# Kernel optimization log

Hardware: AMD Instinct MI355X
Metric: run time of the kernel (lower is better)

The kernel has to match this reference:

```python
import jax, jax.numpy as jnp
import numpy as np

N, D, B, O, E = 4096, 1024, 512, 1, 16  # samples, in_size, bottleneck, out_size, n_tasks
L1_LAMBDA = 1e-4


def setup_inputs() -> dict:
    key = jax.random.key(0)
    ks = jax.random.split(key, 6)
    x = jax.random.normal(ks[0], (N, D), jnp.float32)
    keys = jax.random.randint(ks[1], (N,), 0, E, dtype=jnp.int32)
    W1 = jax.random.normal(ks[2], (E, B, D), jnp.float32) / np.sqrt(D).astype(np.float32)
    b1 = jax.random.normal(ks[3], (E, B), jnp.float32) * 0.01
    W2 = jax.random.normal(ks[4], (E, O, B), jnp.float32) / np.sqrt(B).astype(np.float32)
    b2 = jax.random.normal(ks[5], (E, O), jnp.float32) * 0.01
    return {"x": x, "keys": keys, "W1": W1, "b1": b1, "W2": W2, "b2": b2}


def reference(x, keys, W1, b1, W2, b2):
    """Per-sample task-specific 2-layer bottleneck MLP dispatch.

    x: [N, D] float; keys: [N] int task indices.
    W1: [E, B, D], b1: [E, B], W2: [E, O, B], b2: [E, O].
    Returns (out [N, O], l1_lambda * sum_n L1(params of expert keys[n])).
    """
    n = x.shape[0]
    e = W1.shape[0]
    # Dense MoE dispatch: first linear for all experts, then select per sample.
    h_all = jnp.einsum('nd,ebd->neb', x, W1) + b1[None]          # [N, E, B]
    h = h_all[jnp.arange(n), keys]                                # [N, B]
    h = jax.nn.relu(h)                                            # activation='relu'
    out = jnp.einsum('nb,nob->no', h, W2[keys]) + b2[keys]        # [N, O]
    # L1 of the selected expert's parameters is accumulated once per sample.
    l1_per_expert = (jnp.abs(W1).sum((1, 2)) + jnp.abs(b1).sum(1)
                     + jnp.abs(W2).sum((1, 2)) + jnp.abs(b2).sum(1))  # [E]
    counts = jnp.zeros((e,), x.dtype).at[keys].add(jnp.ones((), x.dtype))
    l1 = jnp.asarray(L1_LAMBDA, x.dtype) * jnp.dot(counts, l1_per_expert)
    return out, l1
```

## Files before the change

### kernel.cpp

```cpp
#include <hip/hip_runtime.h>
#include <hip/hip_bf16.h>

#define N_S 4096
#define D_IN 1024
#define B_BOT 512
#define E_EXP 16
#define L1_LAMBDA 1e-4f

#define MT 64
#define NT 128
#define KC 64
#define MT_GRID 6
#define IDSTR 512

typedef float f32x4 __attribute__((ext_vector_type(4)));
typedef short bf16x8 __attribute__((ext_vector_type(8)));
typedef unsigned int u32;


__device__ __forceinline__ ushort4 cvt4(float4 v) {
    union { __hip_bfloat162 b2[2]; ushort4 u4; } u;
    u.b2[0] = __float22bfloat162_rn({v.x, v.y});
    u.b2[1] = __float22bfloat162_rn({v.z, v.w});
    return u.u4;
}

__device__ __forceinline__ void async16(const ushort* g, ushort* l) {
    __builtin_amdgcn_global_load_lds(
        (const __attribute__((address_space(1))) u32*)g,
        (__attribute__((address_space(3))) u32*)l, 16, 0, 0);
}

__global__ __launch_bounds__(256)
void prep_kernel(const float* __restrict__ x, const int* __restrict__ keys,
                 const float* __restrict__ W1, const float* __restrict__ b1,
                 const float* __restrict__ W2, const float* __restrict__ b2,
                 float* __restrict__ out, int* __restrict__ counts,
                 float* __restrict__ l1small, float* __restrict__ l1part,
                 int* __restrict__ ids, ushort* __restrict__ W1b,
                 ushort* __restrict__ xb) {
    const int blk = blockIdx.x;
    const int t = threadIdx.x;
    if (blk < E_EXP) {
        const int e = blk;
        out[e * 256 + t] = 0.f;
        float s = fabsf(b1[e * B_BOT + t]) + fabsf(b1[e * B_BOT + 256 + t])
                + fabsf(W2[e * B_BOT + t]) + fabsf(W2[e * B_BOT + 256 + t]);
        if (t == 0) s += fabsf(b2[e]);
#pragma unroll
        for (int off = 32; off > 0; off >>= 1) s += __shfl_down(s, off);
        __shared__ float ws4a[4];
        __shared__ int cnt_s;
        if ((t & 63) == 0) ws4a[t >> 6] = s;
        if (t == 0) cnt_s = 0;
        __syncthreads();
        if (t == 0) l1small[e] = ws4a[0] + ws4a[1] + ws4a[2] + ws4a[3];
        const int lane = t & 63;
        for (int it = 0; it < N_S / 256; ++it) {
            const int i = it * 256 + t;
            const bool m = (keys[i] == e);
            const unsigned long long mask = __ballot(m);
            int base = 0;
            if (lane == 0) base = atomicAdd(&cnt_s, __popcll(mask));
            base = __shfl(base, 0);
            if (m) {
                const int pos = base + __popcll(mask & ((1ull << lane) - 1ull));
                if (pos < IDSTR) ids[e * IDSTR + pos] = i;
            }
        }
        __syncthreads();
        if (t == 0) counts[e] = min(cnt_s, IDSTR);
    } else if (blk < E_EXP + 1024) {
        const int i = blk - E_EXP;
        const long long base = (long long)i * 2048;
        const float4* __restrict__ src = (const float4*)W1;
        ushort4* __restrict__ dst = (ushort4*)W1b;
        float s = 0.f;
#pragma unroll
        for (int m = 0; m < 8; ++m) {
            const long long idx = base + m * 256 + t;
            float4 v = src[idx];
            s += fabsf(v.x) + fabsf(v.y) + fabsf(v.z) + fabsf(v.w);
            dst[idx] = cvt4(v);
        }
#pragma unroll
        for (int off = 32; off > 0; off >>= 1) s += __shfl_down(s, off);
        __shared__ float ws4b[4];
        if ((t & 63) == 0) ws4b[t >> 6] = s;
        __syncthreads();
        if (t == 0) l1part[i] = ws4b[0] + ws4b[1] + ws4b[2] + ws4b[3];
    } else {
        const int i = blk - E_EXP - 1024;
        const long long base = (long long)i * 2048;
        const float4* __restrict__ src = (const float4*)x;
        ushort4* __restrict__ dst = (ushort4*)xb;
#pragma unroll
        for (int m = 0; m < 8; ++m) {
            const long long idx = base + m * 256 + t;
            dst[idx] = cvt4(src[idx]);
        }
    }
}

__global__ __launch_bounds__(256, 2)
void mlp_kernel(const ushort* __restrict__ W1b, const ushort* __restrict__ xb,
                const float* __restrict__ b1, const float* __restrict__ W2,
                const float* __restrict__ b2, const int* __restrict__ counts,
                const float* __restrict__ l1small, const float* __restrict__ l1part,
                const int* __restrict__ ids, float* __restrict__ out) {
    const int b = blockIdx.x;
    const int mt = b >> 6, e = (b & 63) >> 2, nb = b & 3;
    const int t = threadIdx.x, wave = t >> 6, lane = t & 63;
    const int l15 = lane & 15, qd = lane >> 4;
    const int wm = wave & 1, wn = wave >> 1;

    __shared__ __align__(16) ushort As[MT * KC];
    __shared__ __align__(16) ushort Bs[NT * KC];
    __shared__ int sid_s[MT];
    __shared__ float red[2][MT];

    if (b == 0 && wave == 0) {
        const int el = lane >> 2, sub = lane & 3;
        float s = 0.f;
#pragma unroll
        for (int k = 0; k < 16; ++k) s += l1part[el * 64 + sub * 16 + k];
        s += __shfl_xor(s, 1);
        s += __shfl_xor(s, 2);
        float v = (sub == 0) ? (float)counts[el] * (s + l1small[el]) : 0.f;
        v += __shfl_xor(v, 4);
        v += __shfl_xor(v, 8);
        v += __shfl_xor(v, 16);
        v += __shfl_xor(v, 32);
        if (lane == 0) out[N_S] = L1_LAMBDA * v;
    }

    const int cnt = counts[e];
    const int m0 = mt * MT;
    if (m0 >= cnt) return;

    if (t < MT) sid_s[t] = ids[e * IDSTR + min(m0 + t, cnt - 1)];
    __syncthreads();

    const int colb = nb * NT;
    float b1v[4], w2v[4];
#pragma unroll
    for (int j = 0; j < 4; ++j) {
        const int col = colb + 64 * wn + 16 * j + l15;
        b1v[j] = b1[e * B_BOT + col];
        w2v[j] = W2[e * B_BOT + col];
    }
    const float b2e = b2[e];

    const ushort* gA[2];
    ushort* dA[2];
#pragma unroll
    for (int p = 0; p < 2; ++p) {
        const int u = p * 256 + t, r = u >> 3;
        const int q = (u & 7) ^ (r & 7);
        gA[p] = xb + (size_t)sid_s[r] * D_IN + q * 8;
        dA[p] = As + (size_t)(p * 256 + wave * 64) * 8;
    }
    const ushort* gB[4];
    ushort* dB[4];
#pragma unroll
    for (int p = 0; p < 4; ++p) {
        const int u = p * 256 + t, r = u >> 3;
        const int q = (u & 7) ^ (r & 7);
        gB[p] = W1b + (size_t)(e * B_BOT + colb + r) * D_IN + q * 8;
        dB[p] = Bs + (size_t)(p * 256 + wave * 64) * 8;
    }

    const ushort* fA[2][2];
#pragma unroll
    for (int i = 0; i < 2; ++i)
#pragma unroll
        for (int s = 0; s < 2; ++s) {
            const int r = 32 * wm + 16 * i + l15;
            fA[i][s] = As + (size_t)(r * 8 + ((s * 4 + qd) ^ (r & 7))) * 8;
        }
    const ushort* fB[4][2];
#pragma unroll
    for (int j = 0; j < 4; ++j)
#pragma unroll
        for (int s = 0; s < 2; ++s) {
            const int r = 64 * wn + 16 * j + l15;
            fB[j][s] = Bs + (size_t)(r * 8 + ((s * 4 + qd) ^ (r & 7))) * 8;
        }

    f32x4 acc[2][4];
#pragma unroll
    for (int i = 0; i < 2; ++i)
#pragma unroll
        for (int j = 0; j < 4; ++j) acc[i][j] = (f32x4){0.f, 0.f, 0.f, 0.f};

    for (int c = 0; c < D_IN / KC; ++c) {
        const int ko = c * KC;
        __syncthreads();
#pragma unroll
        for (int p = 0; p < 2; ++p) async16(gA[p] + ko, dA[p]);
#pragma unroll
        for (int p = 0; p < 4; ++p) async16(gB[p] + ko, dB[p]);
        __syncthreads();
#pragma unroll
        for (int s = 0; s < 2; ++s) {
            bf16x8 a0 = *(const bf16x8*)fA[0][s];
            bf16x8 a1 = *(const bf16x8*)fA[1][s];
            bf16x8 bb[4];
#pragma unroll
            for (int j = 0; j < 4; ++j) bb[j] = *(const bf16x8*)fB[j][s];
#pragma unroll
            for (int j = 0; j < 4; ++j) {
                acc[0][j] = __builtin_amdgcn_mfma_f32_16x16x32_bf16(a0, bb[j], acc[0][j], 0, 0, 0);
                acc[1][j] = __builtin_amdgcn_mfma_f32_16x16x32_bf16(a1, bb[j], acc[1][j], 0, 0, 0);
            }
        }
    }

    float p[2][4] = {{0.f, 0.f, 0.f, 0.f}, {0.f, 0.f, 0.f, 0.f}};
#pragma unroll
    for (int j = 0; j < 4; ++j)
#pragma unroll
        for (int i = 0; i < 2; ++i)
#pragma unroll
            for (int r = 0; r < 4; ++r) {
                const float h = fmaxf(acc[i][j][r] + b1v[j], 0.f);
                p[i][r] = fmaf(h, w2v[j], p[i][r]);
            }
#pragma unroll
    for (int off = 8; off > 0; off >>= 1)
#pragma unroll
        for (int i = 0; i < 2; ++i)
#pragma unroll
            for (int r = 0; r < 4; ++r) p[i][r] += __shfl_xor(p[i][r], off, 16);

    if (l15 == 0) {
#pragma unroll
        for (int i = 0; i < 2; ++i)
#pragma unroll
            for (int r = 0; r < 4; ++r)
                red[wn][32 * wm + 16 * i + 4 * qd + r] = p[i][r];
    }
    __syncthreads();
    if (t < MT) {
        const int m = m0 + t;
        if (m < cnt) {
            float v = red[0][t] + red[1][t];
            if (nb == 0) v += b2e;
            atomicAdd(&out[ids[e * IDSTR + m]], v);
        }
    }
}

extern "C" void kernel_launch(void* const* d_in, const int* in_sizes, int n_in,
                              void* d_out, int out_size, void* d_ws, size_t ws_size,
                              hipStream_t stream) {
    const float* x    = (const float*)d_in[0];
    const int*   keys = (const int*)d_in[1];
    const float* W1   = (const float*)d_in[2];
    const float* b1   = (const float*)d_in[3];
    const float* W2   = (const float*)d_in[4];
    const float* b2   = (const float*)d_in[5];
    float* out = (float*)d_out;

    char* ws = (char*)d_ws;
    int*    counts  = (int*)(ws + 0);
    float*  l1small = (float*)(ws + 64);
    float*  l1part  = (float*)(ws + 128);
    int*    ids     = (int*)(ws + 4224);
    ushort* W1b     = (ushort*)(ws + 65536);
    ushort* xb      = (ushort*)(ws + 65536 + 16777216);

    prep_kernel<<<E_EXP + 1024 + 512, 256, 0, stream>>>(
        x, keys, W1, b1, W2, b2, out, counts, l1small, l1part, ids, W1b, xb);
    mlp_kernel<<<MT_GRID * 64, 256, 0, stream>>>(
        W1b, xb, b1, W2, b2, counts, l1small, l1part, ids, out);
}
```

Before: 115.7 us.

## Double-buffer LDS tiles to overlap async global loads with MFMA compute

```diff
diff --git a/kernel.cpp b/kernel.cpp
--- a/kernel.cpp
+++ b/kernel.cpp
@@ -114,8 +114,10 @@
     const int l15 = lane & 15, qd = lane >> 4;
     const int wm = wave & 1, wn = wave >> 1;
 
-    __shared__ __align__(16) ushort As[MT * KC];
-    __shared__ __align__(16) ushort Bs[NT * KC];
+    __shared__ __align__(16) ushort As0[MT * KC];
+    __shared__ __align__(16) ushort As1[MT * KC];
+    __shared__ __align__(16) ushort Bs0[NT * KC];
+    __shared__ __align__(16) ushort Bs1[NT * KC];
     __shared__ int sid_s[MT];
     __shared__ float red[2][MT];
 
@@ -152,39 +154,37 @@
     const float b2e = b2[e];
 
     const ushort* gA[2];
-    ushort* dA[2];
+    const int dldsA[2] = {(0 * 256 + wave * 64) * 8, (1 * 256 + wave * 64) * 8};
 #pragma unroll
     for (int p = 0; p < 2; ++p) {
         const int u = p * 256 + t, r = u >> 3;
         const int q = (u & 7) ^ (r & 7);
         gA[p] = xb + (size_t)sid_s[r] * D_IN + q * 8;
-        dA[p] = As + (size_t)(p * 256 + wave * 64) * 8;
     }
     const ushort* gB[4];
-    ushort* dB[4];
+    int dldsB[4];
 #pragma unroll
     for (int p = 0; p < 4; ++p) {
         const int u = p * 256 + t, r = u >> 3;
         const int q = (u & 7) ^ (r & 7);
         gB[p] = W1b + (size_t)(e * B_BOT + colb + r) * D_IN + q * 8;
-        dB[p] = Bs + (size_t)(p * 256 + wave * 64) * 8;
-    }
-
-    const ushort* fA[2][2];
+        dldsB[p] = (p * 256 + wave * 64) * 8;
+    }
+
+    int offA[2][2], offB[4][2];
 #pragma unroll
     for (int i = 0; i < 2; ++i)
 #pragma unroll
         for (int s = 0; s < 2; ++s) {
             const int r = 32 * wm + 16 * i + l15;
-            fA[i][s] = As + (size_t)(r * 8 + ((s * 4 + qd) ^ (r & 7))) * 8;
-        }
-    const ushort* fB[4][2];
+            offA[i][s] = (r * 8 + ((s * 4 + qd) ^ (r & 7))) * 8;
+        }
 #pragma unroll
     for (int j = 0; j < 4; ++j)
 #pragma unroll
         for (int s = 0; s < 2; ++s) {
             const int r = 64 * wn + 16 * j + l15;
-            fB[j][s] = Bs + (size_t)(r * 8 + ((s * 4 + qd) ^ (r & 7))) * 8;
+            offB[j][s] = (r * 8 + ((s * 4 + qd) ^ (r & 7))) * 8;
         }
 
     f32x4 acc[2][4];
@@ -193,28 +193,50 @@
 #pragma unroll
         for (int j = 0; j < 4; ++j) acc[i][j] = (f32x4){0.f, 0.f, 0.f, 0.f};
 
-    for (int c = 0; c < D_IN / KC; ++c) {
-        const int ko = c * KC;
-        __syncthreads();
-#pragma unroll
-        for (int p = 0; p < 2; ++p) async16(gA[p] + ko, dA[p]);
-#pragma unroll
-        for (int p = 0; p < 4; ++p) async16(gB[p] + ko, dB[p]);
-        __syncthreads();
-#pragma unroll
-        for (int s = 0; s < 2; ++s) {
-            bf16x8 a0 = *(const bf16x8*)fA[0][s];
-            bf16x8 a1 = *(const bf16x8*)fA[1][s];
-            bf16x8 bb[4];
-#pragma unroll
-            for (int j = 0; j < 4; ++j) bb[j] = *(const bf16x8*)fB[j][s];
-#pragma unroll
-            for (int j = 0; j < 4; ++j) {
-                acc[0][j] = __builtin_amdgcn_mfma_f32_16x16x32_bf16(a0, bb[j], acc[0][j], 0, 0, 0);
-                acc[1][j] = __builtin_amdgcn_mfma_f32_16x16x32_bf16(a1, bb[j], acc[1][j], 0, 0, 0);
-            }
-        }
-    }
+#define STAGE(ko, Ad, Bd)                                         \
+    do {                                                          \
+        _Pragma("unroll")                                         \
+        for (int p = 0; p < 2; ++p)                               \
+            async16(gA[p] + (ko), (Ad) + dldsA[p]);               \
+        _Pragma("unroll")                                         \
+        for (int p = 0; p < 4; ++p)                               \
+            async16(gB[p] + (ko), (Bd) + dldsB[p]);               \
+    } while (0)
+
+#define COMPUTE(Ab, Bb)                                                        \
+    do {                                                                       \
+        _Pragma("unroll")                                                      \
+        for (int s = 0; s < 2; ++s) {                                          \
+            bf16x8 a0 = *(const bf16x8*)((Ab) + offA[0][s]);                   \
+            bf16x8 a1 = *(const bf16x8*)((Ab) + offA[1][s]);                   \
+            bf16x8 bb[4];                                                      \
+            _Pragma("unroll")                                                  \
+            for (int j = 0; j < 4; ++j)                                        \
+                bb[j] = *(const bf16x8*)((Bb) + offB[j][s]);                   \
+            _Pragma("unroll")                                                  \
+            for (int j = 0; j < 4; ++j) {                                      \
+                acc[0][j] = __builtin_amdgcn_mfma_f32_16x16x32_bf16(           \
+                    a0, bb[j], acc[0][j], 0, 0, 0);                            \
+                acc[1][j] = __builtin_amdgcn_mfma_f32_16x16x32_bf16(           \
+                    a1, bb[j], acc[1][j], 0, 0, 0);                            \
+            }                                                                  \
+        }                                                                      \
+    } while (0)
+
+    STAGE(0, As0, Bs0);
+    __syncthreads();
+
+#pragma unroll 1
+    for (int c = 0; c < D_IN / KC; c += 2) {
+        if (c + 1 < D_IN / KC) STAGE((c + 1) * KC, As1, Bs1);
+        COMPUTE(As0, Bs0);
+        __syncthreads();
+        if (c + 2 < D_IN / KC) STAGE((c + 2) * KC, As0, Bs0);
+        COMPUTE(As1, Bs1);
+        __syncthreads();
+    }
+#undef STAGE
+#undef COMPUTE
 
     float p[2][4] = {{0.f, 0.f, 0.f, 0.f}, {0.f, 0.f, 0.f, 0.f}};
 #pragma unroll
```

New measurement: 112.6 us. -2.7%, faster.
